# Kernel optimization log

Measured on AMD Instinct MI355X. Metric: run time of the kernel, lower is better.

## Reference

```python
import jax, jax.numpy as jnp
import numpy as np

B, N, D = 16, 4096, 256
S = 8            # num_slots
ITERS = 3
H = 256          # mlp hidden = max(dim, 256)
SCALE = D ** -0.5
TEMP = 1.0
LN_EPS = 1e-5


def _ln(x, g, b):
    mu = jnp.mean(x, axis=-1, keepdims=True)
    var = jnp.var(x, axis=-1, keepdims=True)
    return (x - mu) * jax.lax.rsqrt(var + LN_EPS) * g + b


def setup_inputs() -> dict:
    key = jax.random.key(0)
    ks = jax.random.split(key, 16)
    xav = float(np.sqrt(6.0 / (S * D + D)))  # xavier_uniform over (1,S,D)
    lin = float(np.sqrt(1.0 / D))
    return {
        "embeddings": jax.random.normal(ks[0], (B, N, D), jnp.float32),
        "slots_noise": jax.random.normal(ks[1], (1, S, D), jnp.float32) * 0.0 + jax.random.normal(ks[1], (B, S, D), jnp.float32),
        "slots_mu": jax.random.uniform(ks[2], (1, S, D), jnp.float32, -xav, xav),
        "slots_logsigma": jax.random.uniform(ks[3], (1, S, D), jnp.float32, -xav, xav),
        "Wk": jax.random.uniform(ks[4], (S, D, D), jnp.float32, -lin, lin),
        "Wq": jax.random.uniform(ks[5], (D, D), jnp.float32, -lin, lin),
        "Wv": jax.random.uniform(ks[6], (S, D, D), jnp.float32, -lin, lin),
        "W_ih": jax.random.uniform(ks[7], (3 * D, D), jnp.float32, -lin, lin),
        "W_hh": jax.random.uniform(ks[8], (3 * D, D), jnp.float32, -lin, lin),
        "b_ih": jax.random.uniform(ks[9], (3 * D,), jnp.float32, -lin, lin),
        "b_hh": jax.random.uniform(ks[10], (3 * D,), jnp.float32, -lin, lin),
        "W1": jax.random.uniform(ks[11], (H, D), jnp.float32, -lin, lin),
        "b1": jnp.zeros((H,), jnp.float32),
        "W2": jax.random.uniform(ks[12], (D, H), jnp.float32, -float(np.sqrt(1.0 / H)), float(np.sqrt(1.0 / H))),
        "b2": jnp.zeros((D,), jnp.float32),
        "g_in": jnp.ones((D,), jnp.float32), "be_in": jnp.zeros((D,), jnp.float32),
        "g_s": jnp.ones((D,), jnp.float32), "be_s": jnp.zeros((D,), jnp.float32),
        "g_ff": jnp.ones((D,), jnp.float32), "be_ff": jnp.zeros((D,), jnp.float32),
    }


def _gru(x, h, W_ih, W_hh, b_ih, b_hh):
    # torch.nn.GRUCell math; x,h: [M, D]
    gi = x @ W_ih.T + b_ih
    gh = h @ W_hh.T + b_hh
    i_r, i_z, i_n = jnp.split(gi, 3, axis=-1)
    h_r, h_z, h_n = jnp.split(gh, 3, axis=-1)
    r = jax.nn.sigmoid(i_r + h_r)
    z = jax.nn.sigmoid(i_z + h_z)
    n = jnp.tanh(i_n + r * h_n)
    return (1.0 - z) * n + z * h


def reference(embeddings, slots_noise, slots_mu, slots_logsigma, Wk, Wq, Wv,
              W_ih, W_hh, b_ih, b_hh, W1, b1, W2, b2,
              g_in, be_in, g_s, be_s, g_ff, be_ff):
    b, n, d = embeddings.shape
    slots = slots_mu + jnp.exp(slots_logsigma) * slots_noise   # [B,S,D]
    emb = _ln(embeddings, g_in, be_in)                          # [B,N,D]
    # per-slot keys / values: keys[s] = emb @ Wk[s].T  -> [S,B,N,D]
    keys = jnp.einsum('bnd,sed->sbne', emb, Wk)
    values = jnp.einsum('bnd,sed->sbne', emb, Wv)

    attn_vis = None
    for _ in range(ITERS):
        slots_prev = slots
        slots_n = _ln(slots, g_s, be_s)
        q = jnp.einsum('bsd,ed->bse', slots_n, Wq)              # [B,S,D]
        dots = jnp.einsum('bsd,sbnd->bsn', q, keys) * SCALE     # [B,S,N]
        attn = jax.nn.softmax(dots / TEMP, axis=1)              # softmax over slots
        attn_vis = attn
        attn_w = attn / jnp.sum(attn, axis=-1, keepdims=True)   # normalize over tokens
        updates = jnp.einsum('sbnd,bsn->bsd', values, attn_w)   # [B,S,D]
        h = _gru(updates.reshape(b * S, d), slots_prev.reshape(b * S, d),
                 W_ih, W_hh, b_ih, b_hh).reshape(b, S, d)
        ff = _ln(h, g_ff, be_ff)
        slots = h + (jax.nn.relu(ff @ W1.T + b1) @ W2.T + b2)
    return slots, attn_vis
```

## Files before the change

### kernel.cpp

```cpp
#include <hip/hip_runtime.h>
#include <hip/hip_bf16.h>

typedef unsigned short u16;
typedef unsigned int u32;

#define DEVI __device__ __forceinline__

constexpr float SCALE = 0.0625f;
constexpr float LN_EPS = 1e-5f;

DEVI float dot8f(const float* __restrict__ w, const float* __restrict__ x){
  float4 a = *(const float4*)w;
  float4 b = *(const float4*)(w + 4);
  return a.x*x[0]+a.y*x[1]+a.z*x[2]+a.w*x[3]+b.x*x[4]+b.y*x[5]+b.z*x[6]+b.w*x[7];
}

__global__ void k_init_slots(const float* __restrict__ noise, const float* __restrict__ smu,
                             const float* __restrict__ slsig, float* __restrict__ slots){
  const int r = blockIdx.x, tid = threadIdx.x;
  const int s = r & 7;
  slots[r*256 + tid] = smu[s*256 + tid] + expf(slsig[s*256 + tid]) * noise[r*256 + tid];
}

__global__ __launch_bounds__(256) void k_qg(const float* __restrict__ slots,
    const float* __restrict__ Wq, const float* __restrict__ Wk,
    const float* __restrict__ g_s, const float* __restrict__ be_s,
    const float* __restrict__ g_in, const float* __restrict__ be_in,
    float* __restrict__ qg, float* __restrict__ gqbq,
    float* __restrict__ uacc, float* __restrict__ Zacc){
  __shared__ float partQ[256][33];
  __shared__ float partK[8][256];
  __shared__ float sn[256];
  __shared__ float qv[256];
  __shared__ float red[8];
  const int r = blockIdx.x, tid = threadIdx.x;
  const int s = r & 7;
  const int lane = tid & 63, wv = tid >> 6;
  uacc[r*256 + tid] = 0.f;
  if (tid == 0) Zacc[r] = 0.f;
  float x = slots[r*256 + tid];
  float v1 = x, v2 = x*x;
  #pragma unroll
  for (int o = 32; o; o >>= 1){ v1 += __shfl_xor(v1,o,64); v2 += __shfl_xor(v2,o,64); }
  if (lane == 0){ red[wv] = v1; red[4+wv] = v2; }
  __syncthreads();
  {
    float mu = (red[0]+red[1]+red[2]+red[3]) * (1.f/256.f);
    float var = (red[4]+red[5]+red[6]+red[7]) * (1.f/256.f) - mu*mu;
    float inv = rsqrtf(var + LN_EPS);
    sn[tid] = (x - mu)*inv*g_s[tid] + be_s[tid];
  }
  __syncthreads();
  const int c8 = tid & 31, ep = tid >> 5;
  {
    float xs8[8];
    #pragma unroll
    for (int j = 0; j < 8; ++j) xs8[j] = sn[c8*8 + j];
    const float* Wb = Wq + c8*8;
    #pragma unroll 4
    for (int ei = 0; ei < 32; ++ei){
      int e = ep*32 + ei;
      partQ[e][c8] = dot8f(Wb + (size_t)e*256, xs8);
    }
  }
  __syncthreads();
  {
    float acc = 0.f;
    #pragma unroll
    for (int p = 0; p < 32; ++p) acc += partQ[tid][p];
    qv[tid] = acc;
  }
  __syncthreads();
  {
    float acc8[8];
    #pragma unroll
    for (int j = 0; j < 8; ++j) acc8[j] = 0.f;
    const float* Wb = Wk + ((size_t)s*256)*256 + c8*8;
    #pragma unroll 4
    for (int ei = 0; ei < 32; ++ei){
      int e = ep*32 + ei;
      const float* wp = Wb + (size_t)e*256;
      float4 wa = *(const float4*)wp;
      float4 wb = *(const float4*)(wp + 4);
      float qe = qv[e];
      acc8[0] += qe*wa.x; acc8[1] += qe*wa.y; acc8[2] += qe*wa.z; acc8[3] += qe*wa.w;
      acc8[4] += qe*wb.x; acc8[5] += qe*wb.y; acc8[6] += qe*wb.z; acc8[7] += qe*wb.w;
    }
    float* pk = &partK[ep][c8*8];
    #pragma unroll
    for (int j = 0; j < 8; ++j) pk[j] = acc8[j];
  }
  __syncthreads();
  {
    float qk = 0.f;
    #pragma unroll
    for (int p = 0; p < 8; ++p) qk += partK[p][tid];
    float qgv = qk * g_in[tid] * SCALE;
    float bqv = qk * be_in[tid] * SCALE;
    qg[r*256 + tid] = qgv;
    float vq = qgv, vb = bqv;
    #pragma unroll
    for (int o = 32; o; o >>= 1){ vq += __shfl_xor(vq,o,64); vb += __shfl_xor(vb,o,64); }
    if (lane == 0){ red[wv] = vq; red[4+wv] = vb; }
  }
  __syncthreads();
  if (tid == 0) gqbq[r*2+0] = red[0]+red[1]+red[2]+red[3];
  if (tid == 1) gqbq[r*2+1] = red[4]+red[5]+red[6]+red[7];
}

__global__ __launch_bounds__(256) void k_main(const float* __restrict__ emb,
    const float* __restrict__ qg, const float* __restrict__ gqbq,
    const float* __restrict__ g_in, const float* __restrict__ be_in,
    float* __restrict__ uacc, float* __restrict__ Zacc,
    float* __restrict__ out_attn, int write_attn){
  __shared__ __align__(16) float Xs[32*260];
  __shared__ float qgL[8*256];
  __shared__ float aL[8*32];
  __shared__ float avL[8*32];
  __shared__ float muL[32], invL[32];
  __shared__ float Wred[2][8][4];
  __shared__ float Zs[8], A2s[8], GqL[8], BqL[8];

  const int tid = threadIdx.x;
  const int lane = tid & 63;
  const int wv = tid >> 6;
  const int blk = blockIdx.x;
  const int b = blk >> 7;
  const int tile = blk & 127;
  const int n0 = tile * 32;

  {
    const float4* src = (const float4*)(qg + (size_t)b * 2048);
    float4* dst = (float4*)qgL;
    dst[tid] = src[tid];
    dst[tid + 256] = src[tid + 256];
  }
  if (tid < 8){
    GqL[tid] = gqbq[(b*8 + tid)*2 + 0];
    BqL[tid] = gqbq[(b*8 + tid)*2 + 1];
  }
  {
    const float4* src = (const float4*)(emb + ((size_t)b*4096 + n0) * 256);
    #pragma unroll
    for (int k = 0; k < 8; ++k){
      int v = tid + 256*k;
      float4 u = src[v];
      int t = v >> 6;
      int c0 = (v & 63) * 4;
      *(float4*)(&Xs[t*260 + c0]) = u;
    }
  }
  __syncthreads();

  const int t = tid >> 3;
  const int qq = tid & 7;
  {
    const float4* xp = (const float4*)(&Xs[t*260 + qq*32]);
    float s1 = 0.f, s2 = 0.f;
    #pragma unroll
    for (int j = 0; j < 8; ++j){
      float4 u = xp[j];
      s1 += (u.x+u.y)+(u.z+u.w);
      s2 += u.x*u.x+u.y*u.y+u.z*u.z+u.w*u.w;
    }
    s1 += __shfl_xor(s1, 1, 64); s2 += __shfl_xor(s2, 1, 64);
    s1 += __shfl_xor(s1, 2, 64); s2 += __shfl_xor(s2, 2, 64);
    s1 += __shfl_xor(s1, 4, 64); s2 += __shfl_xor(s2, 4, 64);
    if (qq == 0){
      float mu = s1 * (1.f/256.f);
      float var = s2 * (1.f/256.f) - mu*mu;
      muL[t] = mu;
      invL[t] = rsqrtf(var + LN_EPS);
    }
  }
  __syncthreads();
  {
    float acc[8];
    #pragma unroll
    for (int s = 0; s < 8; ++s) acc[s] = 0.f;
    const float4* xp = (const float4*)(&Xs[t*260 + qq*32]);
    #pragma unroll 2
    for (int j = 0; j < 8; ++j){
      float4 u = xp[j];
      const float* qb = &qgL[qq*32 + j*4];
      #pragma unroll
      for (int s = 0; s < 8; ++s){
        float4 q0 = *(const float4*)(qb + s*256);
        acc[s] += u.x*q0.x + u.y*q0.y + u.z*q0.z + u.w*q0.w;
      }
    }
    #pragma unroll
    for (int s = 0; s < 8; ++s){
      acc[s] += __shfl_xor(acc[s], 1, 64);
      acc[s] += __shfl_xor(acc[s], 2, 64);
      acc[s] += __shfl_xor(acc[s], 4, 64);
    }
    float mu = muL[t], inv = invL[t];
    float dv[8], mx = -1e30f;
    #pragma unroll
    for (int s = 0; s < 8; ++s){
      dv[s] = inv * (acc[s] - mu * GqL[s]) + BqL[s];
      mx = fmaxf(mx, dv[s]);
    }
    float den = 0.f;
    #pragma unroll
    for (int s = 0; s < 8; ++s){ dv[s] = expf(dv[s] - mx); den += dv[s]; }
    float rden = 1.f / den;
    #pragma unroll
    for (int s = 0; s < 8; ++s){
      float at = dv[s] * rden;
      float av = at * inv;
      if (qq == 0){ avL[s*32 + t] = at; aL[s*32 + t] = av; }
      float z1 = at, z2 = av * mu;
      #pragma unroll
      for (int o = 32; o; o >>= 1){ z1 += __shfl_xor(z1, o, 64); z2 += __shfl_xor(z2, o, 64); }
      if (lane == 0){ Wred[0][s][wv] = z1 * 0.125f; Wred[1][s][wv] = z2 * 0.125f; }
    }
  }
  __syncthreads();
  if (tid < 8){
    Zs[tid]  = Wred[0][tid][0]+Wred[0][tid][1]+Wred[0][tid][2]+Wred[0][tid][3];
    A2s[tid] = Wred[1][tid][0]+Wred[1][tid][1]+Wred[1][tid][2]+Wred[1][tid][3];
  }
  if (write_attn){
    int s = tid >> 5, tk = tid & 31;
    out_attn[((size_t)(b*8 + s))*4096 + n0 + tk] = avL[s*32 + tk];
  }
  __syncthreads();
  {
    const int c = tid;
    float S1[8];
    #pragma unroll
    for (int s = 0; s < 8; ++s) S1[s] = 0.f;
    #pragma unroll 2
    for (int t4 = 0; t4 < 8; ++t4){
      float x0 = Xs[(t4*4+0)*260 + c];
      float x1 = Xs[(t4*4+1)*260 + c];
      float x2 = Xs[(t4*4+2)*260 + c];
      float x3 = Xs[(t4*4+3)*260 + c];
      #pragma unroll
      for (int s = 0; s < 8; ++s){
        float4 a4 = *(const float4*)(&aL[s*32 + t4*4]);
        S1[s] += x0*a4.x + x1*a4.y + x2*a4.z + x3*a4.w;
      }
    }
    float gc = g_in[c];
    float bc = be_in[c];
    float* dst = uacc + ((size_t)b*8)*256 + c;
    #pragma unroll
    for (int s = 0; s < 8; ++s){
      atomicAdd(&dst[s*256], gc * (S1[s] - A2s[s]) + bc * Zs[s]);
    }
    if (tid < 8) atomicAdd(&Zacc[b*8 + tid], Zs[tid]);
  }
}

__global__ __launch_bounds__(256) void k_updates(const float* __restrict__ uacc, const float* __restrict__ Zacc,
    const float* __restrict__ Wv, float* __restrict__ upd){
  __shared__ float part[256][33];
  __shared__ float uL[256];
  const int r = blockIdx.x, tid = threadIdx.x;
  const int s = r & 7;
  uL[tid] = uacc[r*256 + tid];
  __syncthreads();
  const float rz = 1.f / Zacc[r];
  const int c8 = tid & 31, dp = tid >> 5;
  float xs8[8];
  #pragma unroll
  for (int j = 0; j < 8; ++j) xs8[j] = uL[c8*8 + j];
  const float* Wb = Wv + ((size_t)s*256)*256 + c8*8;
  #pragma unroll 4
  for (int di = 0; di < 32; ++di){
    int d = dp*32 + di;
    part[d][c8] = dot8f(Wb + (size_t)d*256, xs8);
  }
  __syncthreads();
  float acc = 0.f;
  #pragma unroll
  for (int p = 0; p < 32; ++p) acc += part[tid][p];
  upd[r*256 + tid] = acc * rz;
}

__global__ __launch_bounds__(256) void k_gruGemv(const float* __restrict__ upd, const float* __restrict__ slots,
    const float* __restrict__ W_ih, const float* __restrict__ W_hh,
    const float* __restrict__ b_ih, const float* __restrict__ b_hh,
    float* __restrict__ gigh){
  __shared__ float xL[256];
  __shared__ float part[256][33];
  const int which = blockIdx.x;
  const int r = blockIdx.y;
  const int tid = threadIdx.x;
  const int g = (which < 3) ? which : which - 3;
  const float* xsrc = (which < 3) ? (upd + r*256) : (slots + r*256);
  const float* W = (which < 3) ? W_ih : W_hh;
  const float* bias = (which < 3) ? b_ih : b_hh;
  xL[tid] = xsrc[tid];
  __syncthreads();
  const int c8 = tid & 31, dp = tid >> 5;
  float xs8[8];
  #pragma unroll
  for (int j = 0; j < 8; ++j) xs8[j] = xL[c8*8 + j];
  const float* Wb = W + ((size_t)g*256)*256 + c8*8;
  #pragma unroll 4
  for (int di = 0; di < 32; ++di){
    int d = dp*32 + di;
    part[d][c8] = dot8f(Wb + (size_t)d*256, xs8);
  }
  __syncthreads();
  float acc = 0.f;
  #pragma unroll
  for (int p = 0; p < 32; ++p) acc += part[tid][p];
  gigh[((size_t)r*6 + which)*256 + tid] = acc + bias[g*256 + tid];
}

__global__ __launch_bounds__(256) void k_mlp(const float* __restrict__ gigh, float* __restrict__ slots,
    const float* __restrict__ W1, const float* __restrict__ b1,
    const float* __restrict__ W2, const float* __restrict__ b2,
    const float* __restrict__ g_ff, const float* __restrict__ be_ff,
    float* __restrict__ out_slots, int last){
  __shared__ float part[256][33];
  __shared__ float hL[256];
  __shared__ float lnh[256];
  __shared__ float hid[256];
  __shared__ float red[8];
  const int r = blockIdx.x, tid = threadIdx.x;
  const int lane = tid & 63, wv = tid >> 6;
  const float* gg = gigh + (size_t)r*6*256;
  float i_r = gg[tid],     i_z = gg[256+tid],  i_n = gg[512+tid];
  float h_r = gg[768+tid], h_z = gg[1024+tid], h_n = gg[1280+tid];
  float hp = slots[r*256 + tid];
  float rg = 1.f/(1.f + expf(-(i_r + h_r)));
  float zg = 1.f/(1.f + expf(-(i_z + h_z)));
  float ng = tanhf(i_n + rg*h_n);
  float h = (1.f - zg)*ng + zg*hp;
  hL[tid] = h;
  float v1 = h, v2 = h*h;
  #pragma unroll
  for (int o = 32; o; o >>= 1){ v1 += __shfl_xor(v1,o,64); v2 += __shfl_xor(v2,o,64); }
  if (lane == 0){ red[wv] = v1; red[4+wv] = v2; }
  __syncthreads();
  {
    float mu = (red[0]+red[1]+red[2]+red[3]) * (1.f/256.f);
    float var = (red[4]+red[5]+red[6]+red[7]) * (1.f/256.f) - mu*mu;
    float inv = rsqrtf(var + LN_EPS);
    lnh[tid] = (h - mu)*inv*g_ff[tid] + be_ff[tid];
  }
  __syncthreads();
  const int c8 = tid & 31, dp = tid >> 5;
  {
    float xs8[8];
    #pragma unroll
    for (int j = 0; j < 8; ++j) xs8[j] = lnh[c8*8 + j];
    const float* Wb = W1 + c8*8;
    #pragma unroll 4
    for (int di = 0; di < 32; ++di){
      int d = dp*32 + di;
      part[d][c8] = dot8f(Wb + (size_t)d*256, xs8);
    }
  }
  __syncthreads();
  {
    float acc = 0.f;
    #pragma unroll
    for (int p = 0; p < 32; ++p) acc += part[tid][p];
    hid[tid] = fmaxf(acc + b1[tid], 0.f);
  }
  __syncthreads();
  {
    float xs8[8];
    #pragma unroll
    for (int j = 0; j < 8; ++j) xs8[j] = hid[c8*8 + j];
    const float* Wb = W2 + c8*8;
    #pragma unroll 4
    for (int di = 0; di < 32; ++di){
      int d = dp*32 + di;
      part[d][c8] = dot8f(Wb + (size_t)d*256, xs8);
    }
  }
  __syncthreads();
  {
    float acc = 0.f;
    #pragma unroll
    for (int p = 0; p < 32; ++p) acc += part[tid][p];
    float out = hL[tid] + acc + b2[tid];
    slots[r*256 + tid] = out;
    if (last) out_slots[r*256 + tid] = out;
  }
}

extern "C" void kernel_launch(void* const* d_in, const int* in_sizes, int n_in,
                              void* d_out, int out_size, void* d_ws, size_t ws_size,
                              hipStream_t stream){
  const float* emb   = (const float*)d_in[0];
  const float* noise = (const float*)d_in[1];
  const float* smu   = (const float*)d_in[2];
  const float* slsig = (const float*)d_in[3];
  const float* Wk    = (const float*)d_in[4];
  const float* Wq    = (const float*)d_in[5];
  const float* Wv    = (const float*)d_in[6];
  const float* W_ih  = (const float*)d_in[7];
  const float* W_hh  = (const float*)d_in[8];
  const float* b_ih  = (const float*)d_in[9];
  const float* b_hh  = (const float*)d_in[10];
  const float* W1    = (const float*)d_in[11];
  const float* b1    = (const float*)d_in[12];
  const float* W2    = (const float*)d_in[13];
  const float* b2    = (const float*)d_in[14];
  const float* g_in  = (const float*)d_in[15];
  const float* be_in = (const float*)d_in[16];
  const float* g_s   = (const float*)d_in[17];
  const float* be_s  = (const float*)d_in[18];
  const float* g_ff  = (const float*)d_in[19];
  const float* be_ff = (const float*)d_in[20];

  float* ws    = (float*)d_ws;
  float* slots = ws;
  float* qg    = ws + 32768;
  float* gqbq  = ws + 65536;
  float* upd   = ws + 65792;
  float* gigh  = ws + 98560;
  float* uacc  = ws + 295168;
  float* Zacc  = ws + 327936;

  float* out_slots = (float*)d_out;
  float* out_attn  = out_slots + 32768;
  const int has_attn = (out_size >= 32768 + 16*8*4096);

  k_init_slots<<<dim3(128), dim3(256), 0, stream>>>(noise, smu, slsig, slots);
  for (int it = 0; it < 3; ++it){
    int last = (it == 2);
    k_qg<<<dim3(128), dim3(256), 0, stream>>>(slots, Wq, Wk, g_s, be_s, g_in, be_in, qg, gqbq, uacc, Zacc);
    k_main<<<dim3(2048), dim3(256), 0, stream>>>(emb, qg, gqbq, g_in, be_in, uacc, Zacc, out_attn, last && has_attn);
    k_updates<<<dim3(128), dim3(256), 0, stream>>>(uacc, Zacc, Wv, upd);
    k_gruGemv<<<dim3(6,128), dim3(256), 0, stream>>>(upd, slots, W_ih, W_hh, b_ih, b_hh, gigh);
    k_mlp<<<dim3(128), dim3(256), 0, stream>>>(gigh, slots, W1, b1, W2, b2, g_ff, be_ff, out_slots, last);
  }
}
```

Baseline: 401.1 us.

## Fuse per-slot GEMV chain into one kernel and stream embeddings from registers

The separate updates, GRU GEMV, MLP and next-iteration query kernels are merged into one 128-block kernel, and slot init is merged into the first query kernel. This cuts the launch count from 16 to 7 and removes the intermediate upd/gigh buffers. The main attention kernel no longer stages the embedding tile in LDS: it loads each row into registers and rereads columns from global/L2 in the second pass, with a swizzled qg layout to reduce bank conflicts. The cost is that the fused kernel runs eleven GEMVs serially on only 128 blocks, the embedding tile is read twice from memory, and LDS use is lower so occupancy may change.

```diff
diff --git a/kernel.cpp b/kernel.cpp
--- a/kernel.cpp
+++ b/kernel.cpp
@@ -1,8 +1,4 @@
 #include <hip/hip_runtime.h>
-#include <hip/hip_bf16.h>
-
-typedef unsigned short u16;
-typedef unsigned int u32;
 
 #define DEVI __device__ __forceinline__
 
@@ -15,97 +11,103 @@
   return a.x*x[0]+a.y*x[1]+a.z*x[2]+a.w*x[3]+b.x*x[4]+b.y*x[5]+b.z*x[6]+b.w*x[7];
 }
 
-__global__ void k_init_slots(const float* __restrict__ noise, const float* __restrict__ smu,
-                             const float* __restrict__ slsig, float* __restrict__ slots){
-  const int r = blockIdx.x, tid = threadIdx.x;
-  const int s = r & 7;
-  slots[r*256 + tid] = smu[s*256 + tid] + expf(slsig[s*256 + tid]) * noise[r*256 + tid];
-}
-
-__global__ __launch_bounds__(256) void k_qg(const float* __restrict__ slots,
+DEVI float gemv256(const float* __restrict__ W, const float* __restrict__ xv,
+                   float (*part)[33], int tid){
+  const int c8 = tid & 31, dp = tid >> 5;
+  float xs8[8];
+  #pragma unroll
+  for (int j = 0; j < 8; ++j) xs8[j] = xv[c8*8 + j];
+  #pragma unroll 4
+  for (int di = 0; di < 32; ++di){
+    int d = dp*32 + di;
+    part[d][c8] = dot8f(W + (size_t)d*256 + c8*8, xs8);
+  }
+  __syncthreads();
+  float acc = 0.f;
+  #pragma unroll
+  for (int p = 0; p < 32; ++p) acc += part[tid][p];
+  __syncthreads();
+  return acc;
+}
+
+DEVI float block_ln(float x, const float* __restrict__ g, const float* __restrict__ be,
+                    float* red, int tid, int lane, int wv){
+  float v1 = x, v2 = x*x;
+  #pragma unroll
+  for (int o = 32; o; o >>= 1){ v1 += __shfl_xor(v1,o,64); v2 += __shfl_xor(v2,o,64); }
+  if (lane == 0){ red[wv] = v1; red[4+wv] = v2; }
+  __syncthreads();
+  float mu = (red[0]+red[1]+red[2]+red[3]) * (1.f/256.f);
+  float var = (red[4]+red[5]+red[6]+red[7]) * (1.f/256.f) - mu*mu;
+  float inv = rsqrtf(var + LN_EPS);
+  float r = (x - mu)*inv*g[tid] + be[tid];
+  __syncthreads();
+  return r;
+}
+
+DEVI void q_gen(float snew, int r, int s, int tid, int lane, int wv,
+                const float* __restrict__ Wq, const float* __restrict__ Wk,
+                const float* __restrict__ g_s, const float* __restrict__ be_s,
+                const float* __restrict__ g_in, const float* __restrict__ be_in,
+                float* __restrict__ qg, float* __restrict__ gqbq,
+                float* xv, float (*part)[33], float (*partK)[256], float* red){
+  float sn = block_ln(snew, g_s, be_s, red, tid, lane, wv);
+  xv[tid] = sn; __syncthreads();
+  float q = gemv256(Wq, xv, part, tid);
+  xv[tid] = q; __syncthreads();
+  const int c8 = tid & 31, ep = tid >> 5;
+  float acc8[8];
+  #pragma unroll
+  for (int j = 0; j < 8; ++j) acc8[j] = 0.f;
+  const float* Wb = Wk + ((size_t)s*256)*256 + c8*8;
+  #pragma unroll 4
+  for (int ei = 0; ei < 32; ++ei){
+    int e = ep*32 + ei;
+    const float* wp = Wb + (size_t)e*256;
+    float4 wa = *(const float4*)wp;
+    float4 wb = *(const float4*)(wp + 4);
+    float qe = xv[e];
+    acc8[0] += qe*wa.x; acc8[1] += qe*wa.y; acc8[2] += qe*wa.z; acc8[3] += qe*wa.w;
+    acc8[4] += qe*wb.x; acc8[5] += qe*wb.y; acc8[6] += qe*wb.z; acc8[7] += qe*wb.w;
+  }
+  float* pk = &partK[ep][c8*8];
+  #pragma unroll
+  for (int j = 0; j < 8; ++j) pk[j] = acc8[j];
+  __syncthreads();
+  float qk = 0.f;
+  #pragma unroll
+  for (int p = 0; p < 8; ++p) qk += partK[p][tid];
+  float qgv = qk * g_in[tid] * SCALE;
+  float bqv = qk * be_in[tid] * SCALE;
+  qg[r*256 + tid] = qgv;
+  float vq = qgv, vb = bqv;
+  #pragma unroll
+  for (int o = 32; o; o >>= 1){ vq += __shfl_xor(vq,o,64); vb += __shfl_xor(vb,o,64); }
+  if (lane == 0){ red[wv] = vq; red[4+wv] = vb; }
+  __syncthreads();
+  if (tid == 0) gqbq[r*2+0] = red[0]+red[1]+red[2]+red[3];
+  if (tid == 1) gqbq[r*2+1] = red[4]+red[5]+red[6]+red[7];
+}
+
+__global__ __launch_bounds__(256) void k_qg0(const float* __restrict__ noise,
+    const float* __restrict__ smu, const float* __restrict__ slsig,
     const float* __restrict__ Wq, const float* __restrict__ Wk,
     const float* __restrict__ g_s, const float* __restrict__ be_s,
     const float* __restrict__ g_in, const float* __restrict__ be_in,
-    float* __restrict__ qg, float* __restrict__ gqbq,
+    float* __restrict__ slots, float* __restrict__ qg, float* __restrict__ gqbq,
     float* __restrict__ uacc, float* __restrict__ Zacc){
-  __shared__ float partQ[256][33];
+  __shared__ float part[256][33];
   __shared__ float partK[8][256];
-  __shared__ float sn[256];
-  __shared__ float qv[256];
+  __shared__ float xv[256];
   __shared__ float red[8];
   const int r = blockIdx.x, tid = threadIdx.x;
-  const int s = r & 7;
-  const int lane = tid & 63, wv = tid >> 6;
+  const int s = r & 7, lane = tid & 63, wv = tid >> 6;
+  float x = smu[s*256 + tid] + expf(slsig[s*256 + tid]) * noise[r*256 + tid];
+  slots[r*256 + tid] = x;
   uacc[r*256 + tid] = 0.f;
   if (tid == 0) Zacc[r] = 0.f;
-  float x = slots[r*256 + tid];
-  float v1 = x, v2 = x*x;
-  #pragma unroll
-  for (int o = 32; o; o >>= 1){ v1 += __shfl_xor(v1,o,64); v2 += __shfl_xor(v2,o,64); }
-  if (lane == 0){ red[wv] = v1; red[4+wv] = v2; }
-  __syncthreads();
-  {
-    float mu = (red[0]+red[1]+red[2]+red[3]) * (1.f/256.f);
-    float var = (red[4]+red[5]+red[6]+red[7]) * (1.f/256.f) - mu*mu;
-    float inv = rsqrtf(var + LN_EPS);
-    sn[tid] = (x - mu)*inv*g_s[tid] + be_s[tid];
-  }
-  __syncthreads();
-  const int c8 = tid & 31, ep = tid >> 5;
-  {
-    float xs8[8];
-    #pragma unroll
-    for (int j = 0; j < 8; ++j) xs8[j] = sn[c8*8 + j];
-    const float* Wb = Wq + c8*8;
-    #pragma unroll 4
-    for (int ei = 0; ei < 32; ++ei){
-      int e = ep*32 + ei;
-      partQ[e][c8] = dot8f(Wb + (size_t)e*256, xs8);
-    }
-  }
-  __syncthreads();
-  {
-    float acc = 0.f;
-    #pragma unroll
-    for (int p = 0; p < 32; ++p) acc += partQ[tid][p];
-    qv[tid] = acc;
-  }
-  __syncthreads();
-  {
-    float acc8[8];
-    #pragma unroll
-    for (int j = 0; j < 8; ++j) acc8[j] = 0.f;
-    const float* Wb = Wk + ((size_t)s*256)*256 + c8*8;
-    #pragma unroll 4
-    for (int ei = 0; ei < 32; ++ei){
-      int e = ep*32 + ei;
-      const float* wp = Wb + (size_t)e*256;
-      float4 wa = *(const float4*)wp;
-      float4 wb = *(const float4*)(wp + 4);
-      float qe = qv[e];
-      acc8[0] += qe*wa.x; acc8[1] += qe*wa.y; acc8[2] += qe*wa.z; acc8[3] += qe*wa.w;
-      acc8[4] += qe*wb.x; acc8[5] += qe*wb.y; acc8[6] += qe*wb.z; acc8[7] += qe*wb.w;
-    }
-    float* pk = &partK[ep][c8*8];
-    #pragma unroll
-    for (int j = 0; j < 8; ++j) pk[j] = acc8[j];
-  }
-  __syncthreads();
-  {
-    float qk = 0.f;
-    #pragma unroll
-    for (int p = 0; p < 8; ++p) qk += partK[p][tid];
-    float qgv = qk * g_in[tid] * SCALE;
-    float bqv = qk * be_in[tid] * SCALE;
-    qg[r*256 + tid] = qgv;
-    float vq = qgv, vb = bqv;
-    #pragma unroll
-    for (int o = 32; o; o >>= 1){ vq += __shfl_xor(vq,o,64); vb += __shfl_xor(vb,o,64); }
-    if (lane == 0){ red[wv] = vq; red[4+wv] = vb; }
-  }
-  __syncthreads();
-  if (tid == 0) gqbq[r*2+0] = red[0]+red[1]+red[2]+red[3];
-  if (tid == 1) gqbq[r*2+1] = red[4]+red[5]+red[6]+red[7];
+  q_gen(x, r, s, tid, lane, wv, Wq, Wk, g_s, be_s, g_in, be_in, qg, gqbq,
+        xv, part, partK, red);
 }
 
 __global__ __launch_bounds__(256) void k_main(const float* __restrict__ emb,
@@ -113,76 +115,47 @@
     const float* __restrict__ g_in, const float* __restrict__ be_in,
     float* __restrict__ uacc, float* __restrict__ Zacc,
     float* __restrict__ out_attn, int write_attn){
-  __shared__ __align__(16) float Xs[32*260];
-  __shared__ float qgL[8*256];
-  __shared__ float aL[8*32];
-  __shared__ float avL[8*32];
-  __shared__ float muL[32], invL[32];
+  __shared__ float qgL[2048];
+  __shared__ float aL[256], avL[256];
   __shared__ float Wred[2][8][4];
   __shared__ float Zs[8], A2s[8], GqL[8], BqL[8];
 
-  const int tid = threadIdx.x;
-  const int lane = tid & 63;
-  const int wv = tid >> 6;
-  const int blk = blockIdx.x;
-  const int b = blk >> 7;
-  const int tile = blk & 127;
+  const int tid = threadIdx.x, lane = tid & 63, wv = tid >> 6;
+  const int blk = blockIdx.x, b = blk >> 7, tile = blk & 127;
   const int n0 = tile * 32;
 
   {
     const float4* src = (const float4*)(qg + (size_t)b * 2048);
     float4* dst = (float4*)qgL;
-    dst[tid] = src[tid];
-    dst[tid + 256] = src[tid + 256];
+    #pragma unroll
+    for (int k = 0; k < 2; ++k){
+      int w = tid + k*256;
+      int s = w >> 6, f = w & 63, qq = f >> 3, j = f & 7;
+      dst[s*64 + qq*8 + ((j + qq) & 7)] = src[w];
+    }
   }
   if (tid < 8){
     GqL[tid] = gqbq[(b*8 + tid)*2 + 0];
     BqL[tid] = gqbq[(b*8 + tid)*2 + 1];
   }
-  {
-    const float4* src = (const float4*)(emb + ((size_t)b*4096 + n0) * 256);
-    #pragma unroll
-    for (int k = 0; k < 8; ++k){
-      int v = tid + 256*k;
-      float4 u = src[v];
-      int t = v >> 6;
-      int c0 = (v & 63) * 4;
-      *(float4*)(&Xs[t*260 + c0]) = u;
-    }
-  }
   __syncthreads();
 
   const int t = tid >> 3;
   const int qq = tid & 7;
   {
-    const float4* xp = (const float4*)(&Xs[t*260 + qq*32]);
-    float s1 = 0.f, s2 = 0.f;
+    const float4* xrow = (const float4*)(emb + ((size_t)(b*4096 + n0 + t))*256 + qq*32);
+    float4 xv4[8];
+    #pragma unroll
+    for (int j = 0; j < 8; ++j) xv4[j] = xrow[j];
+    float s1 = 0.f, s2 = 0.f, acc[8];
+    #pragma unroll
+    for (int s = 0; s < 8; ++s) acc[s] = 0.f;
     #pragma unroll
     for (int j = 0; j < 8; ++j){
-      float4 u = xp[j];
+      float4 u = xv4[j];
       s1 += (u.x+u.y)+(u.z+u.w);
       s2 += u.x*u.x+u.y*u.y+u.z*u.z+u.w*u.w;
-    }
-    s1 += __shfl_xor(s1, 1, 64); s2 += __shfl_xor(s2, 1, 64);
-    s1 += __shfl_xor(s1, 2, 64); s2 += __shfl_xor(s2, 2, 64);
-    s1 += __shfl_xor(s1, 4, 64); s2 += __shfl_xor(s2, 4, 64);
-    if (qq == 0){
-      float mu = s1 * (1.f/256.f);
-      float var = s2 * (1.f/256.f) - mu*mu;
-      muL[t] = mu;
-      invL[t] = rsqrtf(var + LN_EPS);
-    }
-  }
-  __syncthreads();
-  {
-    float acc[8];
-    #pragma unroll
-    for (int s = 0; s < 8; ++s) acc[s] = 0.f;
-    const float4* xp = (const float4*)(&Xs[t*260 + qq*32]);
-    #pragma unroll 2
-    for (int j = 0; j < 8; ++j){
-      float4 u = xp[j];
-      const float* qb = &qgL[qq*32 + j*4];
+      const float* qb = qgL + qq*32 + ((j + qq) & 7)*4;
       #pragma unroll
       for (int s = 0; s < 8; ++s){
         float4 q0 = *(const float4*)(qb + s*256);
@@ -190,12 +163,14 @@
       }
     }
     #pragma unroll
-    for (int s = 0; s < 8; ++s){
-      acc[s] += __shfl_xor(acc[s], 1, 64);
-      acc[s] += __shfl_xor(acc[s], 2, 64);
-      acc[s] += __shfl_xor(acc[s], 4, 64);
-    }
-    float mu = muL[t], inv = invL[t];
+    for (int o = 1; o <= 4; o <<= 1){
+      s1 += __shfl_xor(s1,o,64); s2 += __shfl_xor(s2,o,64);
+      #pragma unroll
+      for (int s = 0; s < 8; ++s) acc[s] += __shfl_xor(acc[s],o,64);
+    }
+    float mu = s1 * (1.f/256.f);
+    float var = s2 * (1.f/256.f) - mu*mu;
+    float inv = rsqrtf(var + LN_EPS);
     float dv[8], mx = -1e30f;
     #pragma unroll
     for (int s = 0; s < 8; ++s){
@@ -229,23 +204,23 @@
   __syncthreads();
   {
     const int c = tid;
+    const float* xcol = emb + ((size_t)(b*4096 + n0))*256 + c;
     float S1[8];
     #pragma unroll
     for (int s = 0; s < 8; ++s) S1[s] = 0.f;
     #pragma unroll 2
     for (int t4 = 0; t4 < 8; ++t4){
-      float x0 = Xs[(t4*4+0)*260 + c];
-      float x1 = Xs[(t4*4+1)*260 + c];
-      float x2 = Xs[(t4*4+2)*260 + c];
-      float x3 = Xs[(t4*4+3)*260 + c];
+      float x0 = xcol[(t4*4+0)*256];
+      float x1 = xcol[(t4*4+1)*256];
+      float x2 = xcol[(t4*4+2)*256];
+      float x3 = xcol[(t4*4+3)*256];
       #pragma unroll
       for (int s = 0; s < 8; ++s){
         float4 a4 = *(const float4*)(&aL[s*32 + t4*4]);
         S1[s] += x0*a4.x + x1*a4.y + x2*a4.z + x3*a4.w;
       }
     }
-    float gc = g_in[c];
-    float bc = be_in[c];
+    float gc = g_in[c], bc = be_in[c];
     float* dst = uacc + ((size_t)b*8)*256 + c;
     #pragma unroll
     for (int s = 0; s < 8; ++s){
@@ -255,137 +230,63 @@
   }
 }
 
-__global__ __launch_bounds__(256) void k_updates(const float* __restrict__ uacc, const float* __restrict__ Zacc,
-    const float* __restrict__ Wv, float* __restrict__ upd){
-  __shared__ float part[256][33];
-  __shared__ float uL[256];
-  const int r = blockIdx.x, tid = threadIdx.x;
-  const int s = r & 7;
-  uL[tid] = uacc[r*256 + tid];
-  __syncthreads();
-  const float rz = 1.f / Zacc[r];
-  const int c8 = tid & 31, dp = tid >> 5;
-  float xs8[8];
-  #pragma unroll
-  for (int j = 0; j < 8; ++j) xs8[j] = uL[c8*8 + j];
-  const float* Wb = Wv + ((size_t)s*256)*256 + c8*8;
-  #pragma unroll 4
-  for (int di = 0; di < 32; ++di){
-    int d = dp*32 + di;
-    part[d][c8] = dot8f(Wb + (size_t)d*256, xs8);
-  }
-  __syncthreads();
-  float acc = 0.f;
-  #pragma unroll
-  for (int p = 0; p < 32; ++p) acc += part[tid][p];
-  upd[r*256 + tid] = acc * rz;
-}
-
-__global__ __launch_bounds__(256) void k_gruGemv(const float* __restrict__ upd, const float* __restrict__ slots,
+__global__ __launch_bounds__(256) void k_fused(
+    float* __restrict__ slots, float* __restrict__ uacc, float* __restrict__ Zacc,
+    const float* __restrict__ Wv,
     const float* __restrict__ W_ih, const float* __restrict__ W_hh,
     const float* __restrict__ b_ih, const float* __restrict__ b_hh,
-    float* __restrict__ gigh){
-  __shared__ float xL[256];
-  __shared__ float part[256][33];
-  const int which = blockIdx.x;
-  const int r = blockIdx.y;
-  const int tid = threadIdx.x;
-  const int g = (which < 3) ? which : which - 3;
-  const float* xsrc = (which < 3) ? (upd + r*256) : (slots + r*256);
-  const float* W = (which < 3) ? W_ih : W_hh;
-  const float* bias = (which < 3) ? b_ih : b_hh;
-  xL[tid] = xsrc[tid];
-  __syncthreads();
-  const int c8 = tid & 31, dp = tid >> 5;
-  float xs8[8];
-  #pragma unroll
-  for (int j = 0; j < 8; ++j) xs8[j] = xL[c8*8 + j];
-  const float* Wb = W + ((size_t)g*256)*256 + c8*8;
-  #pragma unroll 4
-  for (int di = 0; di < 32; ++di){
-    int d = dp*32 + di;
-    part[d][c8] = dot8f(Wb + (size_t)d*256, xs8);
-  }
-  __syncthreads();
-  float acc = 0.f;
-  #pragma unroll
-  for (int p = 0; p < 32; ++p) acc += part[tid][p];
-  gigh[((size_t)r*6 + which)*256 + tid] = acc + bias[g*256 + tid];
-}
-
-__global__ __launch_bounds__(256) void k_mlp(const float* __restrict__ gigh, float* __restrict__ slots,
     const float* __restrict__ W1, const float* __restrict__ b1,
     const float* __restrict__ W2, const float* __restrict__ b2,
     const float* __restrict__ g_ff, const float* __restrict__ be_ff,
+    const float* __restrict__ Wq, const float* __restrict__ Wk,
+    const float* __restrict__ g_s, const float* __restrict__ be_s,
+    const float* __restrict__ g_in, const float* __restrict__ be_in,
+    float* __restrict__ qg, float* __restrict__ gqbq,
     float* __restrict__ out_slots, int last){
   __shared__ float part[256][33];
-  __shared__ float hL[256];
-  __shared__ float lnh[256];
-  __shared__ float hid[256];
+  __shared__ float partK[8][256];
+  __shared__ float xv[256];
   __shared__ float red[8];
+  __shared__ float zsh;
   const int r = blockIdx.x, tid = threadIdx.x;
-  const int lane = tid & 63, wv = tid >> 6;
-  const float* gg = gigh + (size_t)r*6*256;
-  float i_r = gg[tid],     i_z = gg[256+tid],  i_n = gg[512+tid];
-  float h_r = gg[768+tid], h_z = gg[1024+tid], h_n = gg[1280+tid];
+  const int s = r & 7, lane = tid & 63, wv = tid >> 6;
+
+  float u = uacc[r*256 + tid];
+  uacc[r*256 + tid] = 0.f;
+  if (tid == 0){ zsh = Zacc[r]; Zacc[r] = 0.f; }
+  xv[tid] = u;
+  __syncthreads();
+  const float rz = 1.f / zsh;
+  float upd = gemv256(Wv + (size_t)s*65536, xv, part, tid) * rz;
+
+  xv[tid] = upd; __syncthreads();
+  float i_r = gemv256(W_ih,           xv, part, tid) + b_ih[tid];
+  float i_z = gemv256(W_ih +  65536,  xv, part, tid) + b_ih[256 + tid];
+  float i_n = gemv256(W_ih + 131072,  xv, part, tid) + b_ih[512 + tid];
+
   float hp = slots[r*256 + tid];
+  xv[tid] = hp; __syncthreads();
+  float h_r = gemv256(W_hh,           xv, part, tid) + b_hh[tid];
+  float h_z = gemv256(W_hh +  65536,  xv, part, tid) + b_hh[256 + tid];
+  float h_n = gemv256(W_hh + 131072,  xv, part, tid) + b_hh[512 + tid];
+
   float rg = 1.f/(1.f + expf(-(i_r + h_r)));
   float zg = 1.f/(1.f + expf(-(i_z + h_z)));
   float ng = tanhf(i_n + rg*h_n);
-  float h = (1.f - zg)*ng + zg*hp;
-  hL[tid] = h;
-  float v1 = h, v2 = h*h;
-  #pragma unroll
-  for (int o = 32; o; o >>= 1){ v1 += __shfl_xor(v1,o,64); v2 += __shfl_xor(v2,o,64); }
-  if (lane == 0){ red[wv] = v1; red[4+wv] = v2; }
-  __syncthreads();
-  {
-    float mu = (red[0]+red[1]+red[2]+red[3]) * (1.f/256.f);
-    float var = (red[4]+red[5]+red[6]+red[7]) * (1.f/256.f) - mu*mu;
-    float inv = rsqrtf(var + LN_EPS);
-    lnh[tid] = (h - mu)*inv*g_ff[tid] + be_ff[tid];
-  }
-  __syncthreads();
-  const int c8 = tid & 31, dp = tid >> 5;
-  {
-    float xs8[8];
-    #pragma unroll
-    for (int j = 0; j < 8; ++j) xs8[j] = lnh[c8*8 + j];
-    const float* Wb = W1 + c8*8;
-    #pragma unroll 4
-    for (int di = 0; di < 32; ++di){
-      int d = dp*32 + di;
-      part[d][c8] = dot8f(Wb + (size_t)d*256, xs8);
-    }
-  }
-  __syncthreads();
-  {
-    float acc = 0.f;
-    #pragma unroll
-    for (int p = 0; p < 32; ++p) acc += part[tid][p];
-    hid[tid] = fmaxf(acc + b1[tid], 0.f);
-  }
-  __syncthreads();
-  {
-    float xs8[8];
-    #pragma unroll
-    for (int j = 0; j < 8; ++j) xs8[j] = hid[c8*8 + j];
-    const float* Wb = W2 + c8*8;
-    #pragma unroll 4
-    for (int di = 0; di < 32; ++di){
-      int d = dp*32 + di;
-      part[d][c8] = dot8f(Wb + (size_t)d*256, xs8);
-    }
-  }
-  __syncthreads();
-  {
-    float acc = 0.f;
-    #pragma unroll
-    for (int p = 0; p < 32; ++p) acc += part[tid][p];
-    float out = hL[tid] + acc + b2[tid];
-    slots[r*256 + tid] = out;
-    if (last) out_slots[r*256 + tid] = out;
-  }
+  float h  = (1.f - zg)*ng + zg*hp;
+
+  float lnh = block_ln(h, g_ff, be_ff, red, tid, lane, wv);
+  xv[tid] = lnh; __syncthreads();
+  float hid = fmaxf(gemv256(W1, xv, part, tid) + b1[tid], 0.f);
+  xv[tid] = hid; __syncthreads();
+  float out = h + gemv256(W2, xv, part, tid) + b2[tid];
+  slots[r*256 + tid] = out;
+  if (last){
+    out_slots[r*256 + tid] = out;
+    return;
+  }
+  q_gen(out, r, s, tid, lane, wv, Wq, Wk, g_s, be_s, g_in, be_in, qg, gqbq,
+        xv, part, partK, red);
 }
 
 extern "C" void kernel_launch(void* const* d_in, const int* in_sizes, int n_in,
@@ -417,22 +318,21 @@
   float* slots = ws;
   float* qg    = ws + 32768;
   float* gqbq  = ws + 65536;
-  float* upd   = ws + 65792;
-  float* gigh  = ws + 98560;
-  float* uacc  = ws + 295168;
-  float* Zacc  = ws + 327936;
+  float* uacc  = ws + 65792;
+  float* Zacc  = ws + 98560;
 
   float* out_slots = (float*)d_out;
   float* out_attn  = out_slots + 32768;
   const int has_attn = (out_size >= 32768 + 16*8*4096);
 
-  k_init_slots<<<dim3(128), dim3(256), 0, stream>>>(noise, smu, slsig, slots);
+  k_qg0<<<dim3(128), dim3(256), 0, stream>>>(noise, smu, slsig, Wq, Wk,
+      g_s, be_s, g_in, be_in, slots, qg, gqbq, uacc, Zacc);
   for (int it = 0; it < 3; ++it){
     int last = (it == 2);
-    k_qg<<<dim3(128), dim3(256), 0, stream>>>(slots, Wq, Wk, g_s, be_s, g_in, be_in, qg, gqbq, uacc, Zacc);
-    k_main<<<dim3(2048), dim3(256), 0, stream>>>(emb, qg, gqbq, g_in, be_in, uacc, Zacc, out_attn, last && has_attn);
-    k_updates<<<dim3(128), dim3(256), 0, stream>>>(uacc, Zacc, Wv, upd);
-    k_gruGemv<<<dim3(6,128), dim3(256), 0, stream>>>(upd, slots, W_ih, W_hh, b_ih, b_hh, gigh);
-    k_mlp<<<dim3(128), dim3(256), 0, stream>>>(gigh, slots, W1, b1, W2, b2, g_ff, be_ff, out_slots, last);
-  }
-}
+    k_main<<<dim3(2048), dim3(256), 0, stream>>>(emb, qg, gqbq, g_in, be_in,
+        uacc, Zacc, out_attn, last && has_attn);
+    k_fused<<<dim3(128), dim3(256), 0, stream>>>(slots, uacc, Zacc, Wv,
+        W_ih, W_hh, b_ih, b_hh, W1, b1, W2, b2, g_ff, be_ff,
+        Wq, Wk, g_s, be_s, g_in, be_in, qg, gqbq, out_slots, last);
+  }
+}
```

Result: faster. 383.2 us (-4.4%).
